# Optimization experiments

Hardware: AMD Instinct MI355X
Metric: run time of the kernel (lower is better)

The kernel has to match this reference:

```python
import jax, jax.numpy as jnp
import numpy as np

N, E, IN, HID, OUT = 40000, 640000, 128, 512, 256


def setup_inputs() -> dict:
    key = jax.random.key(0)
    ks = jax.random.split(key, 8)
    x = jax.random.normal(ks[0], (N, IN), dtype=jnp.float32)
    edge_index = jax.random.randint(ks[1], (2, E), 0, N, dtype=jnp.int64)
    # SAGEConv params: lin_l (applied to aggregated neighbors, with bias),
    # lin_r (applied to root nodes, no bias) -- PyG defaults.
    def lin(k, fin, fout):
        return jax.random.normal(k, (fin, fout), dtype=jnp.float32) / np.sqrt(fin)
    return {
        "x": x,
        "edge_index": edge_index,
        "W1l": lin(ks[2], IN, HID),
        "b1": jnp.zeros((HID,), jnp.float32),
        "W1r": lin(ks[3], IN, HID),
        "W2l": lin(ks[4], HID, OUT),
        "b2": jnp.zeros((OUT,), jnp.float32),
        "W2r": lin(ks[5], HID, OUT),
    }


def _sage_conv(x, src, dst, Wl, b, Wr):
    n = x.shape[0]
    # gather messages from source nodes, mean-aggregate at destination
    msg = x[src]                                            # [E, F]
    agg = jax.ops.segment_sum(msg, dst, num_segments=n)     # [N, F]
    cnt = jax.ops.segment_sum(jnp.ones((src.shape[0],), x.dtype), dst,
                              num_segments=n)               # [N]
    agg = agg / jnp.maximum(cnt, 1.0)[:, None]
    # out = lin_l(mean_neighbors) + lin_r(x)
    return agg @ Wl + b + x @ Wr


def reference(x, edge_index, W1l, b1, W1r, W2l, b2, W2r):
    src, dst = edge_index[0], edge_index[1]
    h = jax.nn.relu(_sage_conv(x, src, dst, W1l, b1, W1r))
    return _sage_conv(h, src, dst, W2l, b2, W2r)
```

## Files before the change

kernel.cpp:

```cpp
#include <hip/hip_runtime.h>


#define N_NODES 40000
#define N_EDGES 640000
#define F_IN 128
#define F_HID 512
#define F_OUT 256
#define NB_SCAN 157

typedef unsigned short ushort_t;
typedef __attribute__((ext_vector_type(8))) short bf16x8;
typedef __attribute__((ext_vector_type(4))) float floatx4;

__device__ __forceinline__ ushort_t f2bf(float f) {
  union { float f; unsigned int u; } x; x.f = f;
  unsigned int r = (x.u + 0x7FFFu + ((x.u >> 16) & 1u)) >> 16;
  return (ushort_t)r;
}
__device__ __forceinline__ float bf2f(ushort_t u) {
  union { unsigned int u; float f; } x; x.u = ((unsigned int)u) << 16;
  return x.f;
}

__global__ void deg_kernel(const int* __restrict__ ei, int* __restrict__ deg) {
  int e = blockIdx.x * blockDim.x + threadIdx.x;
  if (e < N_EDGES) atomicAdd(&deg[ei[N_EDGES + e]], 1);
}

__global__ void scanA_kernel(const int* __restrict__ deg, int* __restrict__ bsum) {
  __shared__ int sdata[256];
  int i = blockIdx.x * 256 + threadIdx.x;
  sdata[threadIdx.x] = (i < N_NODES) ? deg[i] : 0;
  __syncthreads();
  #pragma unroll
  for (int off = 128; off > 0; off >>= 1) {
    if (threadIdx.x < off) sdata[threadIdx.x] += sdata[threadIdx.x + off];
    __syncthreads();
  }
  if (threadIdx.x == 0) bsum[blockIdx.x] = sdata[0];
}

__global__ void scanB_kernel(const int* __restrict__ bsum, int* __restrict__ boff) {
  __shared__ int buf[2][256];
  int tid = threadIdx.x;
  int v = (tid < NB_SCAN) ? bsum[tid] : 0;
  buf[0][tid] = v;
  __syncthreads();
  int cur = 0;
  #pragma unroll
  for (int off = 1; off < 256; off <<= 1) {
    int val = buf[cur][tid];
    if (tid >= off) val += buf[cur][tid - off];
    buf[cur ^ 1][tid] = val;
    __syncthreads();
    cur ^= 1;
  }
  if (tid < NB_SCAN) boff[tid] = buf[cur][tid] - v;
}

__global__ void scanC_kernel(const int* __restrict__ deg, const int* __restrict__ boff,
                             int* __restrict__ rowptr, int* __restrict__ cursor) {
  __shared__ int buf[2][256];
  int tid = threadIdx.x;
  int i = blockIdx.x * 256 + tid;
  int v = (i < N_NODES) ? deg[i] : 0;
  buf[0][tid] = v;
  __syncthreads();
  int cur = 0;
  #pragma unroll
  for (int off = 1; off < 256; off <<= 1) {
    int val = buf[cur][tid];
    if (tid >= off) val += buf[cur][tid - off];
    buf[cur ^ 1][tid] = val;
    __syncthreads();
    cur ^= 1;
  }
  if (i < N_NODES) {
    int ex = boff[blockIdx.x] + buf[cur][tid] - v;
    rowptr[i] = ex;
    cursor[i] = ex;
    if (i == N_NODES - 1) rowptr[N_NODES] = ex + v;
  }
}

__global__ void fill_kernel(const int* __restrict__ ei, int* __restrict__ cursor,
                            int* __restrict__ col) {
  int e = blockIdx.x * blockDim.x + threadIdx.x;
  if (e < N_EDGES) {
    int d = ei[N_EDGES + e];
    int s = ei[e];
    int pos = atomicAdd(&cursor[d], 1);
    col[pos] = s;
  }
}

__global__ void cvt_x_kernel(const float* __restrict__ x, ushort_t* __restrict__ xb) {
  int i = blockIdx.x * blockDim.x + threadIdx.x;
  const int n4 = (N_NODES * F_IN) / 4;
  if (i < n4) {
    float4 v = ((const float4*)x)[i];
    ushort4 o;
    o.x = f2bf(v.x); o.y = f2bf(v.y); o.z = f2bf(v.z); o.w = f2bf(v.w);
    ((ushort4*)xb)[i] = o;
  }
}

__global__ void wp_kernel(const float* __restrict__ W, ushort_t* __restrict__ Wp,
                          int K, int N, int rowoff, int koff, int KT) {
  int i = blockIdx.x * blockDim.x + threadIdx.x;
  if (i < K * N) {
    int n = i / K, k = i - n * K;
    int ng = rowoff + n, kg = koff + k;
    int gg = ng >> 6, ni = (ng >> 4) & 3, lm = ng & 15;
    int c = kg >> 3, j = kg & 7, t = c >> 2, qk = c & 3;
    size_t dst = (((size_t)(gg * (KT / 32) + t) * 4 + ni) * 64 + qk * 16 + lm) * 8 + j;
    Wp[dst] = f2bf(W[(size_t)k * N + n]);
  }
}

__global__ void biascat_kernel(const float* __restrict__ b2, float* __restrict__ bc) {
  int i = threadIdx.x + blockIdx.x * blockDim.x;
  if (i < 512) bc[i] = (i < 256) ? 0.f : b2[i - 256];
}

__global__ void agg1_kernel(const ushort_t* __restrict__ Xb, ushort_t* __restrict__ Yb,
                            const int* __restrict__ rowptr, const int* __restrict__ colidx) {
  __shared__ int cols[64];
  int n = blockIdx.x, f = threadIdx.x;
  int s = rowptr[n], e = rowptr[n + 1];
  float s0 = 0.f, s1 = 0.f;
  for (int base = s; base < e; base += 64) {
    int cnt = min(64, e - base);
    __syncthreads();
    if (f < cnt) cols[f] = colidx[base + f];
    __syncthreads();
    int j = 0;
    for (; j + 4 <= cnt; j += 4) {
      unsigned int v0 = *(const unsigned int*)(Xb + (size_t)cols[j + 0] * F_IN + 2 * f);
      unsigned int v1 = *(const unsigned int*)(Xb + (size_t)cols[j + 1] * F_IN + 2 * f);
      unsigned int v2 = *(const unsigned int*)(Xb + (size_t)cols[j + 2] * F_IN + 2 * f);
      unsigned int v3 = *(const unsigned int*)(Xb + (size_t)cols[j + 3] * F_IN + 2 * f);
      s0 += bf2f((ushort_t)(v0 & 0xffffu)) + bf2f((ushort_t)(v1 & 0xffffu)) +
            bf2f((ushort_t)(v2 & 0xffffu)) + bf2f((ushort_t)(v3 & 0xffffu));
      s1 += bf2f((ushort_t)(v0 >> 16)) + bf2f((ushort_t)(v1 >> 16)) +
            bf2f((ushort_t)(v2 >> 16)) + bf2f((ushort_t)(v3 >> 16));
    }
    for (; j < cnt; ++j) {
      unsigned int v = *(const unsigned int*)(Xb + (size_t)cols[j] * F_IN + 2 * f);
      s0 += bf2f((ushort_t)(v & 0xffffu));
      s1 += bf2f((ushort_t)(v >> 16));
    }
  }
  float inv = 1.f / fmaxf((float)(e - s), 1.f);
  unsigned int o = (unsigned int)f2bf(s0 * inv) | ((unsigned int)f2bf(s1 * inv) << 16);
  *(unsigned int*)(Yb + (size_t)n * F_IN + 2 * f) = o;
}

__global__ void agg2_kernel(const ushort_t* __restrict__ hl, const float* __restrict__ hr,
                            float* __restrict__ out,
                            const int* __restrict__ rowptr, const int* __restrict__ colidx) {
  __shared__ int cols[128];
  int n = blockIdx.x, f = threadIdx.x;
  int s = rowptr[n], e = rowptr[n + 1];
  float s0 = 0.f, s1 = 0.f;
  for (int base = s; base < e; base += 128) {
    int cnt = min(128, e - base);
    __syncthreads();
    if (f < cnt) cols[f] = colidx[base + f];
    __syncthreads();
    int j = 0;
    for (; j + 4 <= cnt; j += 4) {
      unsigned int v0 = *(const unsigned int*)(hl + (size_t)cols[j + 0] * F_OUT + 2 * f);
      unsigned int v1 = *(const unsigned int*)(hl + (size_t)cols[j + 1] * F_OUT + 2 * f);
      unsigned int v2 = *(const unsigned int*)(hl + (size_t)cols[j + 2] * F_OUT + 2 * f);
      unsigned int v3 = *(const unsigned int*)(hl + (size_t)cols[j + 3] * F_OUT + 2 * f);
      s0 += bf2f((ushort_t)(v0 & 0xffffu)) + bf2f((ushort_t)(v1 & 0xffffu)) +
            bf2f((ushort_t)(v2 & 0xffffu)) + bf2f((ushort_t)(v3 & 0xffffu));
      s1 += bf2f((ushort_t)(v0 >> 16)) + bf2f((ushort_t)(v1 >> 16)) +
            bf2f((ushort_t)(v2 >> 16)) + bf2f((ushort_t)(v3 >> 16));
    }
    for (; j < cnt; ++j) {
      unsigned int v = *(const unsigned int*)(hl + (size_t)cols[j] * F_OUT + 2 * f);
      s0 += bf2f((ushort_t)(v & 0xffffu));
      s1 += bf2f((ushort_t)(v >> 16));
    }
  }
  float inv = 1.f / fmaxf((float)(e - s), 1.f);
  float2 hrv = *(const float2*)(hr + (size_t)n * F_OUT + 2 * f);
  float2 o;
  o.x = s0 * inv + hrv.x;
  o.y = s1 * inv + hrv.y;
  *(float2*)(out + (size_t)n * F_OUT + 2 * f) = o;
}

template <bool TWOPAIR, bool RELU, bool BIAS, bool OUT_BF16, bool SPLITOUT, int KT>
__global__ __launch_bounds__(256) void gemm_mfma(
    const ushort_t* __restrict__ A0, const ushort_t* __restrict__ A1,
    const ushort_t* __restrict__ Wp, const float* __restrict__ bias,
    float* __restrict__ Cf, ushort_t* __restrict__ Cb, int M) {
  const int KH = (KT > 256) ? 256 : KT;
  const int NH = KT / KH;
  const int NKH = KH / 8;
  __shared__ ushort_t Apan[64 * KH];
  const int tid = threadIdx.x;
  const int wave = tid >> 6, lane = tid & 63;
  const int lm = lane & 15, qk = lane >> 4;
  const int bn = blockIdx.x * 256;
  const int bm = blockIdx.y * 64;
  const int K0 = TWOPAIR ? KT / 2 : KT;
  const int K0c = K0 / 8;

  const ushort_t* wpg = Wp + (size_t)(blockIdx.x * 4 + wave) * (KT / 32) * 2048;

  auto stageA = [&](int h) {
    #pragma unroll
    for (int q = 0; q < (64 * NKH) / 256; ++q) {
      int c = tid + q * 256;
      int lc = c & (NKH - 1);
      int row = c / NKH;
      int kc = h * NKH + lc;
      const ushort_t* src = (TWOPAIR && kc >= K0c)
          ? A1 + (size_t)(bm + row) * K0 + (kc - K0c) * 8
          : A0 + (size_t)(bm + row) * K0 + kc * 8;
      bf16x8 v = *(const bf16x8*)src;
      size_t off = ((size_t)(lc * 64 + row) * 16) ^ (size_t)((lc & 7) << 4);
      *(bf16x8*)((char*)Apan + off) = v;
    }
  };

  stageA(0);
  bf16x8 bvA[4], bvB[4];
  #pragma unroll
  for (int ni = 0; ni < 4; ++ni)
    bvA[ni] = *(const bf16x8*)(wpg + (size_t)ni * 512 + lane * 8);
  __syncthreads();

  floatx4 acc[4][4] = {};
  #pragma unroll 1
  for (int h = 0; h < NH; ++h) {
    if (h) {
      __syncthreads();
      stageA(h);
      __syncthreads();
    }
    #pragma unroll 1
    for (int kb = 0; kb < KH; kb += 64) {
      const int t0 = (h * KH + kb) / 32;
      #pragma unroll
      for (int ni = 0; ni < 4; ++ni)
        bvB[ni] = *(const bf16x8*)(wpg + ((size_t)(t0 + 1) * 4 + ni) * 512 + lane * 8);

      bf16x8 av[4];
      const int kc0 = kb / 8 + qk;
      #pragma unroll
      for (int mi = 0; mi < 4; ++mi) {
        size_t off = ((size_t)(kc0 * 64 + mi * 16 + lm) * 16) ^ (size_t)((kc0 & 7) << 4);
        av[mi] = *(const bf16x8*)((char*)Apan + off);
      }
      #pragma unroll
      for (int mi = 0; mi < 4; ++mi)
        #pragma unroll
        for (int ni = 0; ni < 4; ++ni)
          acc[mi][ni] = __builtin_amdgcn_mfma_f32_16x16x32_bf16(
              bvA[ni], av[mi], acc[mi][ni], 0, 0, 0);

      if (h * KH + kb + 64 < KT) {
        #pragma unroll
        for (int ni = 0; ni < 4; ++ni)
          bvA[ni] = *(const bf16x8*)(wpg + ((size_t)(t0 + 2) * 4 + ni) * 512 + lane * 8);
      }

      const int kc1 = kb / 8 + 4 + qk;
      #pragma unroll
      for (int mi = 0; mi < 4; ++mi) {
        size_t off = ((size_t)(kc1 * 64 + mi * 16 + lm) * 16) ^ (size_t)((kc1 & 7) << 4);
        av[mi] = *(const bf16x8*)((char*)Apan + off);
      }
      #pragma unroll
      for (int mi = 0; mi < 4; ++mi)
        #pragma unroll
        for (int ni = 0; ni < 4; ++ni)
          acc[mi][ni] = __builtin_amdgcn_mfma_f32_16x16x32_bf16(
              bvB[ni], av[mi], acc[mi][ni], 0, 0, 0);
    }
  }

  #pragma unroll
  for (int ni = 0; ni < 4; ++ni) {
    int colg = bn + wave * 64 + ni * 16 + qk * 4;
    float4 b4 = {0.f, 0.f, 0.f, 0.f};
    if (BIAS) b4 = *(const float4*)&bias[colg];
    #pragma unroll
    for (int mi = 0; mi < 4; ++mi) {
      int rowg = bm + mi * 16 + lm;
      float v0 = acc[mi][ni][0] + b4.x;
      float v1 = acc[mi][ni][1] + b4.y;
      float v2 = acc[mi][ni][2] + b4.z;
      float v3 = acc[mi][ni][3] + b4.w;
      if (RELU) {
        v0 = fmaxf(v0, 0.f); v1 = fmaxf(v1, 0.f);
        v2 = fmaxf(v2, 0.f); v3 = fmaxf(v3, 0.f);
      }
      if (SPLITOUT) {
        if (colg < 256) {
          ushort4 o = {f2bf(v0), f2bf(v1), f2bf(v2), f2bf(v3)};
          *(ushort4*)&Cb[(size_t)rowg * 256 + colg] = o;
        } else {
          float4 o = {v0, v1, v2, v3};
          *(float4*)&Cf[(size_t)rowg * 256 + (colg - 256)] = o;
        }
      } else if (OUT_BF16) {
        ushort4 o = {f2bf(v0), f2bf(v1), f2bf(v2), f2bf(v3)};
        *(ushort4*)&Cb[(size_t)rowg * 512 + colg] = o;
      } else {
        float4 o = {v0, v1, v2, v3};
        *(float4*)&Cf[(size_t)rowg * 512 + colg] = o;
      }
    }
  }
}

extern "C" void kernel_launch(void* const* d_in, const int* in_sizes, int n_in,
                              void* d_out, int out_size, void* d_ws, size_t ws_size,
                              hipStream_t stream) {
  const float* x = (const float*)d_in[0];
  const int* ei = (const int*)d_in[1];
  const float* W1l = (const float*)d_in[2];
  const float* b1 = (const float*)d_in[3];
  const float* W1r = (const float*)d_in[4];
  const float* W2l = (const float*)d_in[5];
  const float* b2 = (const float*)d_in[6];
  const float* W2r = (const float*)d_in[7];
  float* out = (float*)d_out;

  char* ws = (char*)d_ws;
  size_t off = 0;
  auto alloc = [&](size_t bytes) {
    void* p = ws + off;
    off = (off + bytes + 255) & ~(size_t)255;
    return p;
  };
  int* deg = (int*)alloc((size_t)N_NODES * 4);
  int* rowptr = (int*)alloc((size_t)(N_NODES + 1) * 4);
  int* cursor = (int*)alloc((size_t)N_NODES * 4);
  int* col = (int*)alloc((size_t)N_EDGES * 4);
  int* bsum = (int*)alloc((size_t)NB_SCAN * 4);
  int* boff = (int*)alloc((size_t)NB_SCAN * 4);
  ushort_t* x_bf = (ushort_t*)alloc((size_t)N_NODES * F_IN * 2);
  ushort_t* aggx_bf = (ushort_t*)alloc((size_t)N_NODES * F_IN * 2);
  ushort_t* h_bf = (ushort_t*)alloc((size_t)N_NODES * F_HID * 2);
  ushort_t* hl_bf = (ushort_t*)alloc((size_t)N_NODES * F_OUT * 2);
  float* hr = (float*)alloc((size_t)N_NODES * F_OUT * 4);
  ushort_t* Wp1 = (ushort_t*)alloc((size_t)512 * 256 * 2);
  ushort_t* Wp2 = (ushort_t*)alloc((size_t)512 * 512 * 2);
  float* biascat = (float*)alloc(512 * 4);

  hipMemsetAsync(deg, 0, (size_t)N_NODES * 4, stream);
  deg_kernel<<<(N_EDGES + 255) / 256, 256, 0, stream>>>(ei, deg);
  scanA_kernel<<<NB_SCAN, 256, 0, stream>>>(deg, bsum);
  scanB_kernel<<<1, 256, 0, stream>>>(bsum, boff);
  scanC_kernel<<<NB_SCAN, 256, 0, stream>>>(deg, boff, rowptr, cursor);
  fill_kernel<<<(N_EDGES + 255) / 256, 256, 0, stream>>>(ei, cursor, col);

  cvt_x_kernel<<<(N_NODES * F_IN / 4 + 255) / 256, 256, 0, stream>>>(x, x_bf);
  wp_kernel<<<(F_IN * F_HID + 255) / 256, 256, 0, stream>>>(W1l, Wp1, 128, 512, 0, 0, 256);
  wp_kernel<<<(F_IN * F_HID + 255) / 256, 256, 0, stream>>>(W1r, Wp1, 128, 512, 0, 128, 256);
  wp_kernel<<<(F_HID * F_OUT + 255) / 256, 256, 0, stream>>>(W2l, Wp2, 512, 256, 0, 0, 512);
  wp_kernel<<<(F_HID * F_OUT + 255) / 256, 256, 0, stream>>>(W2r, Wp2, 512, 256, 256, 0, 512);
  biascat_kernel<<<2, 256, 0, stream>>>(b2, biascat);

  agg1_kernel<<<N_NODES, 64, 0, stream>>>(x_bf, aggx_bf, rowptr, col);
  gemm_mfma<true, true, true, true, false, 256>
      <<<dim3(2, N_NODES / 64), 256, 0, stream>>>(
          aggx_bf, x_bf, Wp1, b1, nullptr, h_bf, N_NODES);

  gemm_mfma<false, false, true, false, true, 512>
      <<<dim3(2, N_NODES / 64), 256, 0, stream>>>(
          h_bf, nullptr, Wp2, biascat, hr, hl_bf, N_NODES);
  agg2_kernel<<<N_NODES, 128, 0, stream>>>(hl_bf, hr, out, rowptr, col);
}
```

Baseline: 307.6 us.

## Slice feature columns across blocks and split edges across lanes in aggregation

Both aggregation kernels are rewritten so that each block handles one feature slice (eight slices) for 64 nodes. Each wave processes 16 nodes in turn, and within a wave several lane groups work on different edges of the same node, with the partial sums combined by cross-lane shuffles. The aim is to replace one tiny block per node with wider blocks whose concurrent blocks touch only a narrow column slice of the source features, which should improve cache locality for the random gathers and cut block-launch and sync overhead. In exchange, each gathered row segment is small (32 or 64 bytes per node per slice) and colidx is re-read once per slice.

New measurement: 448.3 us. 45.7% more time.

```diff
diff --git a/kernel.cpp b/kernel.cpp
--- a/kernel.cpp
+++ b/kernel.cpp
@@ -123,74 +123,86 @@
   if (i < 512) bc[i] = (i < 256) ? 0.f : b2[i - 256];
 }
 
-__global__ void agg1_kernel(const ushort_t* __restrict__ Xb, ushort_t* __restrict__ Yb,
-                            const int* __restrict__ rowptr, const int* __restrict__ colidx) {
-  __shared__ int cols[64];
-  int n = blockIdx.x, f = threadIdx.x;
-  int s = rowptr[n], e = rowptr[n + 1];
-  float s0 = 0.f, s1 = 0.f;
-  for (int base = s; base < e; base += 64) {
-    int cnt = min(64, e - base);
-    __syncthreads();
-    if (f < cnt) cols[f] = colidx[base + f];
-    __syncthreads();
-    int j = 0;
-    for (; j + 4 <= cnt; j += 4) {
-      unsigned int v0 = *(const unsigned int*)(Xb + (size_t)cols[j + 0] * F_IN + 2 * f);
-      unsigned int v1 = *(const unsigned int*)(Xb + (size_t)cols[j + 1] * F_IN + 2 * f);
-      unsigned int v2 = *(const unsigned int*)(Xb + (size_t)cols[j + 2] * F_IN + 2 * f);
-      unsigned int v3 = *(const unsigned int*)(Xb + (size_t)cols[j + 3] * F_IN + 2 * f);
-      s0 += bf2f((ushort_t)(v0 & 0xffffu)) + bf2f((ushort_t)(v1 & 0xffffu)) +
-            bf2f((ushort_t)(v2 & 0xffffu)) + bf2f((ushort_t)(v3 & 0xffffu));
-      s1 += bf2f((ushort_t)(v0 >> 16)) + bf2f((ushort_t)(v1 >> 16)) +
-            bf2f((ushort_t)(v2 >> 16)) + bf2f((ushort_t)(v3 >> 16));
-    }
-    for (; j < cnt; ++j) {
-      unsigned int v = *(const unsigned int*)(Xb + (size_t)cols[j] * F_IN + 2 * f);
+__global__ __launch_bounds__(256) void agg1_sliced(
+    const ushort_t* __restrict__ Xb, ushort_t* __restrict__ Yb,
+    const int* __restrict__ rowptr, const int* __restrict__ colidx) {
+  const int slice = blockIdx.x & 7;
+  const int g = blockIdx.x >> 3;
+  const int wave = threadIdx.x >> 6, lane = threadIdx.x & 63;
+  const int q = lane >> 3, lm = lane & 7;
+  const int wid = g * 4 + wave;
+  const int colb = slice * 16 + lm * 2;
+  for (int i = 0; i < 16; ++i) {
+    int n = wid * 16 + i;
+    int s = rowptr[n], e = rowptr[n + 1];
+    float s0 = 0.f, s1 = 0.f;
+    int base = s;
+    for (; base + q + 8 < e; base += 16) {
+      int c0 = colidx[base + q];
+      int c1 = colidx[base + q + 8];
+      unsigned int v0 = *(const unsigned int*)(Xb + (size_t)c0 * F_IN + colb);
+      unsigned int v1 = *(const unsigned int*)(Xb + (size_t)c1 * F_IN + colb);
+      s0 += bf2f((ushort_t)(v0 & 0xffffu)) + bf2f((ushort_t)(v1 & 0xffffu));
+      s1 += bf2f((ushort_t)(v0 >> 16)) + bf2f((ushort_t)(v1 >> 16));
+    }
+    for (; base + q < e; base += 8) {
+      int c = colidx[base + q];
+      unsigned int v = *(const unsigned int*)(Xb + (size_t)c * F_IN + colb);
       s0 += bf2f((ushort_t)(v & 0xffffu));
       s1 += bf2f((ushort_t)(v >> 16));
     }
-  }
-  float inv = 1.f / fmaxf((float)(e - s), 1.f);
-  unsigned int o = (unsigned int)f2bf(s0 * inv) | ((unsigned int)f2bf(s1 * inv) << 16);
-  *(unsigned int*)(Yb + (size_t)n * F_IN + 2 * f) = o;
-}
-
-__global__ void agg2_kernel(const ushort_t* __restrict__ hl, const float* __restrict__ hr,
-                            float* __restrict__ out,
-                            const int* __restrict__ rowptr, const int* __restrict__ colidx) {
-  __shared__ int cols[128];
-  int n = blockIdx.x, f = threadIdx.x;
-  int s = rowptr[n], e = rowptr[n + 1];
-  float s0 = 0.f, s1 = 0.f;
-  for (int base = s; base < e; base += 128) {
-    int cnt = min(128, e - base);
-    __syncthreads();
-    if (f < cnt) cols[f] = colidx[base + f];
-    __syncthreads();
-    int j = 0;
-    for (; j + 4 <= cnt; j += 4) {
-      unsigned int v0 = *(const unsigned int*)(hl + (size_t)cols[j + 0] * F_OUT + 2 * f);
-      unsigned int v1 = *(const unsigned int*)(hl + (size_t)cols[j + 1] * F_OUT + 2 * f);
-      unsigned int v2 = *(const unsigned int*)(hl + (size_t)cols[j + 2] * F_OUT + 2 * f);
-      unsigned int v3 = *(const unsigned int*)(hl + (size_t)cols[j + 3] * F_OUT + 2 * f);
-      s0 += bf2f((ushort_t)(v0 & 0xffffu)) + bf2f((ushort_t)(v1 & 0xffffu)) +
-            bf2f((ushort_t)(v2 & 0xffffu)) + bf2f((ushort_t)(v3 & 0xffffu));
-      s1 += bf2f((ushort_t)(v0 >> 16)) + bf2f((ushort_t)(v1 >> 16)) +
-            bf2f((ushort_t)(v2 >> 16)) + bf2f((ushort_t)(v3 >> 16));
-    }
-    for (; j < cnt; ++j) {
-      unsigned int v = *(const unsigned int*)(hl + (size_t)cols[j] * F_OUT + 2 * f);
+    s0 += __shfl_xor(s0, 8);  s1 += __shfl_xor(s1, 8);
+    s0 += __shfl_xor(s0, 16); s1 += __shfl_xor(s1, 16);
+    s0 += __shfl_xor(s0, 32); s1 += __shfl_xor(s1, 32);
+    if (q == 0) {
+      float inv = 1.f / fmaxf((float)(e - s), 1.f);
+      unsigned int o = (unsigned int)f2bf(s0 * inv) |
+                       ((unsigned int)f2bf(s1 * inv) << 16);
+      *(unsigned int*)(Yb + (size_t)n * F_IN + colb) = o;
+    }
+  }
+}
+
+__global__ __launch_bounds__(256) void agg2_sliced(
+    const ushort_t* __restrict__ hl, const float* __restrict__ hr,
+    float* __restrict__ out,
+    const int* __restrict__ rowptr, const int* __restrict__ colidx) {
+  const int slice = blockIdx.x & 7;
+  const int g = blockIdx.x >> 3;
+  const int wave = threadIdx.x >> 6, lane = threadIdx.x & 63;
+  const int q = lane >> 4, lm = lane & 15;
+  const int wid = g * 4 + wave;
+  const int colb = slice * 32 + lm * 2;
+  for (int i = 0; i < 16; ++i) {
+    int n = wid * 16 + i;
+    int s = rowptr[n], e = rowptr[n + 1];
+    float s0 = 0.f, s1 = 0.f;
+    int base = s;
+    for (; base + q + 4 < e; base += 8) {
+      int c0 = colidx[base + q];
+      int c1 = colidx[base + q + 4];
+      unsigned int v0 = *(const unsigned int*)(hl + (size_t)c0 * F_OUT + colb);
+      unsigned int v1 = *(const unsigned int*)(hl + (size_t)c1 * F_OUT + colb);
+      s0 += bf2f((ushort_t)(v0 & 0xffffu)) + bf2f((ushort_t)(v1 & 0xffffu));
+      s1 += bf2f((ushort_t)(v0 >> 16)) + bf2f((ushort_t)(v1 >> 16));
+    }
+    for (; base + q < e; base += 4) {
+      int c = colidx[base + q];
+      unsigned int v = *(const unsigned int*)(hl + (size_t)c * F_OUT + colb);
       s0 += bf2f((ushort_t)(v & 0xffffu));
       s1 += bf2f((ushort_t)(v >> 16));
     }
-  }
-  float inv = 1.f / fmaxf((float)(e - s), 1.f);
-  float2 hrv = *(const float2*)(hr + (size_t)n * F_OUT + 2 * f);
-  float2 o;
-  o.x = s0 * inv + hrv.x;
-  o.y = s1 * inv + hrv.y;
-  *(float2*)(out + (size_t)n * F_OUT + 2 * f) = o;
+    s0 += __shfl_xor(s0, 16); s1 += __shfl_xor(s1, 16);
+    s0 += __shfl_xor(s0, 32); s1 += __shfl_xor(s1, 32);
+    if (q == 0) {
+      float inv = 1.f / fmaxf((float)(e - s), 1.f);
+      float2 hrv = *(const float2*)(hr + (size_t)n * F_OUT + colb);
+      float2 o;
+      o.x = s0 * inv + hrv.x;
+      o.y = s1 * inv + hrv.y;
+      *(float2*)(out + (size_t)n * F_OUT + colb) = o;
+    }
+  }
 }
 
 template <bool TWOPAIR, bool RELU, bool BIAS, bool OUT_BF16, bool SPLITOUT, int KT>
@@ -369,7 +381,7 @@
   wp_kernel<<<(F_HID * F_OUT + 255) / 256, 256, 0, stream>>>(W2r, Wp2, 512, 256, 256, 0, 512);
   biascat_kernel<<<2, 256, 0, stream>>>(b2, biascat);
 
-  agg1_kernel<<<N_NODES, 64, 0, stream>>>(x_bf, aggx_bf, rowptr, col);
+  agg1_sliced<<<5000, 256, 0, stream>>>(x_bf, aggx_bf, rowptr, col);
   gemm_mfma<true, true, true, true, false, 256>
       <<<dim3(2, N_NODES / 64), 256, 0, stream>>>(
           aggx_bf, x_bf, Wp1, b1, nullptr, h_bf, N_NODES);
@@ -377,5 +389,5 @@
   gemm_mfma<false, false, true, false, true, 512>
       <<<dim3(2, N_NODES / 64), 256, 0, stream>>>(
           h_bf, nullptr, Wp2, biascat, hr, hl_bf, N_NODES);
-  agg2_kernel<<<N_NODES, 128, 0, stream>>>(hl_bf, hr, out, rowptr, col);
-}
+  agg2_sliced<<<5000, 256, 0, stream>>>(hl_bf, hr, out, rowptr, col);
+}
```
